# Kernel optimization log

Hardware: AMD Instinct MI355X
Metric: run time of the kernel (lower is better)

## Reference

```python
import math
import jax, jax.numpy as jnp
import numpy as np

B, Q, K, D, H, C = 4, 1024, 1024, 256, 8, 32  # batch, q_len, kv_len, model dim, heads, per-head dim


def setup_inputs() -> dict:
    key = jax.random.key(0)
    ks = jax.random.split(key, 9)
    s = 1.0 / math.sqrt(D)
    return {
        "q_x": jax.random.normal(ks[0], (B, Q, D), jnp.float32),
        "kv_x": jax.random.normal(ks[1], (B, K, D), jnp.float32),
        "bias_mask": jax.random.normal(ks[2], (B, 1, 1, K), jnp.float32),
        "bias_pair": jax.random.normal(ks[3], (B, H, Q, K), jnp.float32),
        "wq": jax.random.normal(ks[4], (D, H * C), jnp.float32) * s,
        "wk": jax.random.normal(ks[5], (D, H * C), jnp.float32) * s,
        "wv": jax.random.normal(ks[6], (D, H * C), jnp.float32) * s,
        "wg": jnp.zeros((D, H * C), jnp.float32),  # gating init: weights 0
        "bg": jnp.ones((H * C,), jnp.float32),     # gating init: bias 1
        "wo": jax.random.normal(ks[7], (H * C, D), jnp.float32) * s,
        "bo": jnp.zeros((D,), jnp.float32),
    }


def reference(q_x, kv_x, bias_mask, bias_pair, wq, wk, wv, wg, bg, wo, bo):
    # project and split heads: [B, L, H, C]
    q = (q_x @ wq).reshape(B, Q, H, C) / math.sqrt(C)
    k = (kv_x @ wk).reshape(B, K, H, C)
    v = (kv_x @ wv).reshape(B, K, H, C)
    # scores [B, H, Q, K] with multiple additive biases
    scores = jnp.einsum("bqhc,bkhc->bhqk", q, k) + bias_mask + bias_pair
    a = jax.nn.softmax(scores, axis=-1)
    o = jnp.einsum("bhqk,bkhc->bqhc", a, v).reshape(B, Q, H * C)
    # sigmoid gate from query activations
    g = jax.nn.sigmoid(q_x @ wg + bg)
    o = o * g
    return o @ wo + bo
```

## Files before the change

### kernel.cpp

```cpp
#include <hip/hip_runtime.h>
#include <hip/hip_bf16.h>


typedef short bf16x8 __attribute__((ext_vector_type(8)));
typedef float f32x4 __attribute__((ext_vector_type(4)));

__device__ __forceinline__ unsigned short f2bf(float f) {
  __hip_bfloat16 hb = __float2bfloat16(f);
  return *reinterpret_cast<const unsigned short*>(&hb);
}

__global__ __launch_bounds__(256) void transpose_conv(
    const float* __restrict__ wq, const float* __restrict__ wk,
    const float* __restrict__ wv, const float* __restrict__ wg,
    const float* __restrict__ wo, unsigned short* __restrict__ wt) {
  __shared__ float t[64][65];
  const int widx = blockIdx.x >> 4;
  const int tile = blockIdx.x & 15;
  const float* src = widx == 0 ? wq : widx == 1 ? wk
                     : widx == 2 ? wv : widx == 3 ? wg : wo;
  unsigned short* dst = wt + widx * 65536;
  const int r0 = (tile >> 2) * 64, c0 = (tile & 3) * 64;
  const int tr = threadIdx.x >> 4;
  const int tc4 = (threadIdx.x & 15) * 4;
#pragma unroll
  for (int i = 0; i < 4; ++i) {
    const float4 u = *reinterpret_cast<const float4*>(
        src + (size_t)(r0 + tr + i * 16) * 256 + c0 + tc4);
    t[tr + i * 16][tc4 + 0] = u.x;
    t[tr + i * 16][tc4 + 1] = u.y;
    t[tr + i * 16][tc4 + 2] = u.z;
    t[tr + i * 16][tc4 + 3] = u.w;
  }
  __syncthreads();
#pragma unroll
  for (int i = 0; i < 4; ++i) {
    const int rr = tr + i * 16;
    ushort4 o;
    o.x = f2bf(t[tc4 + 0][rr]);
    o.y = f2bf(t[tc4 + 1][rr]);
    o.z = f2bf(t[tc4 + 2][rr]);
    o.w = f2bf(t[tc4 + 3][rr]);
    *reinterpret_cast<ushort4*>(dst + (size_t)(c0 + rr) * 256 + r0 + tc4) = o;
  }
}

__global__ __launch_bounds__(256) void proj_mfma(
    const float* __restrict__ q_x, const float* __restrict__ kv_x,
    const unsigned short* __restrict__ wt, const float* __restrict__ bg,
    unsigned short* __restrict__ qhb, unsigned short* __restrict__ khb,
    unsigned short* __restrict__ vhb, float* __restrict__ gws) {
  const int side = blockIdx.y;
  const int m0 = blockIdx.x * 16;
  const int lane = threadIdx.x & 63;
  const int n0 = (threadIdx.x >> 6) * 64;
  const int mrow = lane & 15;
  const int quad = lane >> 4;
  const float* X = side ? kv_x : q_x;
  const unsigned short* W0 = wt + (side ? 1 : 0) * 65536;
  const unsigned short* W1 = wt + (side ? 2 : 3) * 65536;
  f32x4 acc0[4], acc1[4];
  const f32x4 z = {0.f, 0.f, 0.f, 0.f};
#pragma unroll
  for (int nt = 0; nt < 4; ++nt) { acc0[nt] = z; acc1[nt] = z; }

  for (int k0 = 0; k0 < 256; k0 += 32) {
    const size_t abase = (size_t)(m0 + mrow) * 256 + k0 + quad * 8;
    const float4 a0 = *reinterpret_cast<const float4*>(X + abase);
    const float4 a1 = *reinterpret_cast<const float4*>(X + abase + 4);
    bf16x8 a;
    a[0] = (short)f2bf(a0.x); a[1] = (short)f2bf(a0.y);
    a[2] = (short)f2bf(a0.z); a[3] = (short)f2bf(a0.w);
    a[4] = (short)f2bf(a1.x); a[5] = (short)f2bf(a1.y);
    a[6] = (short)f2bf(a1.z); a[7] = (short)f2bf(a1.w);
#pragma unroll
    for (int nt = 0; nt < 4; ++nt) {
      const size_t wrow = (size_t)(n0 + nt * 16 + mrow) * 256 + k0 + quad * 8;
      const bf16x8 b0 = *reinterpret_cast<const bf16x8*>(W0 + wrow);
      const bf16x8 b1 = *reinterpret_cast<const bf16x8*>(W1 + wrow);
      acc0[nt] = __builtin_amdgcn_mfma_f32_16x16x32_bf16(a, b0, acc0[nt], 0, 0, 0);
      acc1[nt] = __builtin_amdgcn_mfma_f32_16x16x32_bf16(a, b1, acc1[nt], 0, 0, 0);
    }
  }

  const int b = m0 >> 10;
#pragma unroll
  for (int nt = 0; nt < 4; ++nt) {
    const int n = n0 + nt * 16 + mrow;
    const int h = n >> 5, c = n & 31;
    const float bgv = (side == 0) ? bg[n] : 0.f;
#pragma unroll
    for (int r = 0; r < 4; ++r) {
      const int row = m0 + quad * 4 + r;
      const int qp = row & 1023;
      const size_t o = ((size_t)(b * 8 + h) * 1024 + qp) * 32 + c;
      if (side == 0) {
        qhb[o] = f2bf(acc0[nt][r] * 0.17677669529663689f);
        const float zz = acc1[nt][r] + bgv;
        gws[(size_t)row * 256 + n] = 1.0f / (1.0f + __expf(-zz));
      } else {
        khb[o] = f2bf(acc0[nt][r]);
        vhb[o] = f2bf(acc1[nt][r]);
      }
    }
  }
}

__global__ __launch_bounds__(256) void attn_mfma(
    const unsigned short* __restrict__ qhb,
    const unsigned short* __restrict__ khb,
    const unsigned short* __restrict__ vhb,
    const float* __restrict__ bias_mask,
    const float* __restrict__ bias_pair,
    const float* __restrict__ gws, unsigned short* __restrict__ og) {
  __shared__ unsigned short ks[64 * 40];
  __shared__ unsigned short vsT[32 * 72];
  __shared__ unsigned short ps[64 * 72];
  const int x = blockIdx.x;
  const int b = x >> 7, h = (x >> 4) & 7, q0 = (x & 15) * 64;
  const int tid = threadIdx.x;
  const int wv = tid >> 6, lane = tid & 63, quad = lane >> 4, lr = lane & 15;
  const int bh = b * 8 + h;

  const bf16x8 aq = *reinterpret_cast<const bf16x8*>(
      qhb + ((size_t)bh * 1024 + q0 + wv * 16 + lr) * 32 + quad * 8);

  float m[4], l[4];
  f32x4 oa[2];
  const f32x4 zero4 = {0.f, 0.f, 0.f, 0.f};
  oa[0] = zero4; oa[1] = zero4;
#pragma unroll
  for (int r = 0; r < 4; ++r) { m[r] = -3e30f; l[r] = 0.f; }

  const float* bp = bias_pair + ((size_t)bh * 1024 + q0 + wv * 16) * 1024;
  const float* bm = bias_mask + (size_t)b * 1024;

  for (int kt = 0; kt < 16; ++kt) {
    const int kk0 = kt * 64;
    __syncthreads();
    {
      const unsigned short* ksrc = khb + (size_t)bh * 32768 + kk0 * 32;
      const int row = tid >> 2, c8 = (tid & 3) * 8;
      *reinterpret_cast<bf16x8*>(ks + row * 40 + c8) =
          *reinterpret_cast<const bf16x8*>(ksrc + row * 32 + c8);
      const unsigned short* vsrc = vhb + (size_t)bh * 32768 + kk0 * 32;
      const bf16x8 vv = *reinterpret_cast<const bf16x8*>(vsrc + row * 32 + c8);
#pragma unroll
      for (int i = 0; i < 8; ++i) vsT[(c8 + i) * 72 + row] = (unsigned short)vv[i];
    }
    __syncthreads();

    f32x4 s[4];
    float mk[4];
#pragma unroll
    for (int nt = 0; nt < 4; ++nt) mk[nt] = bm[kk0 + 16 * nt + lr];
#pragma unroll
    for (int nt = 0; nt < 4; ++nt) {
#pragma unroll
      for (int r = 0; r < 4; ++r)
        s[nt][r] = bp[(size_t)(quad * 4 + r) * 1024 + kk0 + 16 * nt + lr] + mk[nt];
      const bf16x8 bk = *reinterpret_cast<const bf16x8*>(
          ks + (16 * nt + lr) * 40 + quad * 8);
      s[nt] = __builtin_amdgcn_mfma_f32_16x16x32_bf16(aq, bk, s[nt], 0, 0, 0);
    }

#pragma unroll
    for (int r = 0; r < 4; ++r) {
      float mx = fmaxf(fmaxf(s[0][r], s[1][r]), fmaxf(s[2][r], s[3][r]));
      mx = fmaxf(mx, __shfl_xor(mx, 1));
      mx = fmaxf(mx, __shfl_xor(mx, 2));
      mx = fmaxf(mx, __shfl_xor(mx, 4));
      mx = fmaxf(mx, __shfl_xor(mx, 8));
      const float mn = fmaxf(m[r], mx);
      const float alpha = __expf(m[r] - mn);
      float rs = 0.f;
#pragma unroll
      for (int nt = 0; nt < 4; ++nt) {
        s[nt][r] = __expf(s[nt][r] - mn);
        rs += s[nt][r];
      }
      rs += __shfl_xor(rs, 1);
      rs += __shfl_xor(rs, 2);
      rs += __shfl_xor(rs, 4);
      rs += __shfl_xor(rs, 8);
      l[r] = l[r] * alpha + rs;
      m[r] = mn;
      oa[0][r] *= alpha;
      oa[1][r] *= alpha;
      const int ri = wv * 16 + quad * 4 + r;
#pragma unroll
      for (int nt = 0; nt < 4; ++nt)
        ps[ri * 72 + 16 * nt + lr] = f2bf(s[nt][r]);
    }
    asm volatile("s_waitcnt lgkmcnt(0)" ::: "memory");

#pragma unroll
    for (int k0i = 0; k0i < 2; ++k0i) {
      const bf16x8 ap = *reinterpret_cast<const bf16x8*>(
          ps + (wv * 16 + lr) * 72 + k0i * 32 + quad * 8);
#pragma unroll
      for (int nt2 = 0; nt2 < 2; ++nt2) {
        const bf16x8 bv = *reinterpret_cast<const bf16x8*>(
            vsT + (nt2 * 16 + lr) * 72 + k0i * 32 + quad * 8);
        oa[nt2] = __builtin_amdgcn_mfma_f32_16x16x32_bf16(ap, bv, oa[nt2], 0, 0, 0);
      }
    }
  }

#pragma unroll
  for (int r = 0; r < 4; ++r) {
    const int qr = q0 + wv * 16 + quad * 4 + r;
    const float inv = 1.0f / l[r];
    const size_t base = ((size_t)b * 1024 + qr) * 256 + h * 32;
#pragma unroll
    for (int nt2 = 0; nt2 < 2; ++nt2) {
      const int c = nt2 * 16 + lr;
      og[base + c] = f2bf(oa[nt2][r] * inv * gws[base + c]);
    }
  }
}

__global__ __launch_bounds__(256) void outproj_mfma(
    const unsigned short* __restrict__ og,
    const unsigned short* __restrict__ wt,
    const float* __restrict__ bo, float* __restrict__ out) {
  const int m0 = blockIdx.x * 16;
  const int lane = threadIdx.x & 63;
  const int n0 = (threadIdx.x >> 6) * 64;
  const int mrow = lane & 15;
  const int quad = lane >> 4;
  const unsigned short* W = wt + 4 * 65536;
  f32x4 acc[4];
  const f32x4 z = {0.f, 0.f, 0.f, 0.f};
#pragma unroll
  for (int nt = 0; nt < 4; ++nt) acc[nt] = z;

  for (int k0 = 0; k0 < 256; k0 += 32) {
    const bf16x8 a = *reinterpret_cast<const bf16x8*>(
        og + (size_t)(m0 + mrow) * 256 + k0 + quad * 8);
#pragma unroll
    for (int nt = 0; nt < 4; ++nt) {
      const bf16x8 b = *reinterpret_cast<const bf16x8*>(
          W + (size_t)(n0 + nt * 16 + mrow) * 256 + k0 + quad * 8);
      acc[nt] = __builtin_amdgcn_mfma_f32_16x16x32_bf16(a, b, acc[nt], 0, 0, 0);
    }
  }

#pragma unroll
  for (int nt = 0; nt < 4; ++nt) {
    const int n = n0 + nt * 16 + mrow;
    const float bov = bo[n];
#pragma unroll
    for (int r = 0; r < 4; ++r) {
      const int row = m0 + quad * 4 + r;
      out[(size_t)row * 256 + n] = acc[nt][r] + bov;
    }
  }
}

extern "C" void kernel_launch(void* const* d_in, const int* in_sizes, int n_in,
                              void* d_out, int out_size, void* d_ws,
                              size_t ws_size, hipStream_t stream) {
  (void)in_sizes; (void)n_in; (void)out_size; (void)ws_size;
  const float* q_x = (const float*)d_in[0];
  const float* kv_x = (const float*)d_in[1];
  const float* bias_mask = (const float*)d_in[2];
  const float* bias_pair = (const float*)d_in[3];
  const float* wq = (const float*)d_in[4];
  const float* wk = (const float*)d_in[5];
  const float* wv = (const float*)d_in[6];
  const float* wg = (const float*)d_in[7];
  const float* bg = (const float*)d_in[8];
  const float* wo = (const float*)d_in[9];
  const float* bo = (const float*)d_in[10];

  char* wsb = (char*)d_ws;
  unsigned short* wt  = (unsigned short*)(wsb);
  unsigned short* qhb = (unsigned short*)(wsb + 655360);
  unsigned short* khb = (unsigned short*)(wsb + 2752512);
  unsigned short* vhb = (unsigned short*)(wsb + 4849664);
  unsigned short* og  = (unsigned short*)(wsb + 6946816);
  float* gws          = (float*)(wsb + 9043968);

  transpose_conv<<<80, 256, 0, stream>>>(wq, wk, wv, wg, wo, wt);
  proj_mfma<<<dim3(256, 2), 256, 0, stream>>>(q_x, kv_x, wt, bg, qhb, khb,
                                              vhb, gws);
  attn_mfma<<<512, 256, 0, stream>>>(qhb, khb, vhb, bias_mask, bias_pair, gws,
                                     og);
  outproj_mfma<<<256, 256, 0, stream>>>(og, wt, bo, (float*)d_out);
}
```

Baseline: 252.7 us.

## Double-buffer K/V tiles and prefetch bias_pair into registers in attention

The attention kernel now keeps two LDS buffers for K and transposed V. It issues the global loads for the next K/V tile and the next bias_pair/bias_mask values into registers at the start of each iteration, so they overlap the current tile's MFMA and softmax work. This also drops one __syncthreads per iteration. The cost is extra register pressure from holding 16 prefetched bias values plus K/V vectors, which could reduce occupancy.

```diff
diff --git a/kernel.cpp b/kernel.cpp
--- a/kernel.cpp
+++ b/kernel.cpp
@@ -113,8 +113,8 @@
     const float* __restrict__ bias_mask,
     const float* __restrict__ bias_pair,
     const float* __restrict__ gws, unsigned short* __restrict__ og) {
-  __shared__ unsigned short ks[64 * 40];
-  __shared__ unsigned short vsT[32 * 72];
+  __shared__ unsigned short ks[2][64 * 40];
+  __shared__ unsigned short vsT[2][32 * 72];
   __shared__ unsigned short ps[64 * 72];
   const int x = blockIdx.x;
   const int b = x >> 7, h = (x >> 4) & 7, q0 = (x & 15) * 64;
@@ -134,33 +134,53 @@
 
   const float* bp = bias_pair + ((size_t)bh * 1024 + q0 + wv * 16) * 1024;
   const float* bm = bias_mask + (size_t)b * 1024;
+  const unsigned short* kbase = khb + (size_t)bh * 32768;
+  const unsigned short* vbase = vhb + (size_t)bh * 32768;
+  const int srow = tid >> 2, sc8 = (tid & 3) * 8;
+
+  {
+    const bf16x8 k0v = *reinterpret_cast<const bf16x8*>(kbase + srow * 32 + sc8);
+    const bf16x8 v0v = *reinterpret_cast<const bf16x8*>(vbase + srow * 32 + sc8);
+    *reinterpret_cast<bf16x8*>(&ks[0][srow * 40 + sc8]) = k0v;
+#pragma unroll
+    for (int i = 0; i < 8; ++i)
+      vsT[0][(sc8 + i) * 72 + srow] = (unsigned short)v0v[i];
+  }
+  float bpr[4][4], mkr[4];
+#pragma unroll
+  for (int nt = 0; nt < 4; ++nt) {
+    mkr[nt] = bm[16 * nt + lr];
+#pragma unroll
+    for (int r = 0; r < 4; ++r)
+      bpr[nt][r] = bp[(size_t)(quad * 4 + r) * 1024 + 16 * nt + lr];
+  }
+  __syncthreads();
 
   for (int kt = 0; kt < 16; ++kt) {
-    const int kk0 = kt * 64;
-    __syncthreads();
-    {
-      const unsigned short* ksrc = khb + (size_t)bh * 32768 + kk0 * 32;
-      const int row = tid >> 2, c8 = (tid & 3) * 8;
-      *reinterpret_cast<bf16x8*>(ks + row * 40 + c8) =
-          *reinterpret_cast<const bf16x8*>(ksrc + row * 32 + c8);
-      const unsigned short* vsrc = vhb + (size_t)bh * 32768 + kk0 * 32;
-      const bf16x8 vv = *reinterpret_cast<const bf16x8*>(vsrc + row * 32 + c8);
-#pragma unroll
-      for (int i = 0; i < 8; ++i) vsT[(c8 + i) * 72 + row] = (unsigned short)vv[i];
-    }
-    __syncthreads();
+    const int cur = kt & 1;
+
+    bf16x8 kn, vn;
+    float bpn[4][4], mkn[4];
+    if (kt < 15) {
+      const int kk1 = (kt + 1) * 64;
+      kn = *reinterpret_cast<const bf16x8*>(kbase + (size_t)(kk1 + srow) * 32 + sc8);
+      vn = *reinterpret_cast<const bf16x8*>(vbase + (size_t)(kk1 + srow) * 32 + sc8);
+#pragma unroll
+      for (int nt = 0; nt < 4; ++nt) {
+        mkn[nt] = bm[kk1 + 16 * nt + lr];
+#pragma unroll
+        for (int r = 0; r < 4; ++r)
+          bpn[nt][r] = bp[(size_t)(quad * 4 + r) * 1024 + kk1 + 16 * nt + lr];
+      }
+    }
 
     f32x4 s[4];
-    float mk[4];
-#pragma unroll
-    for (int nt = 0; nt < 4; ++nt) mk[nt] = bm[kk0 + 16 * nt + lr];
 #pragma unroll
     for (int nt = 0; nt < 4; ++nt) {
 #pragma unroll
-      for (int r = 0; r < 4; ++r)
-        s[nt][r] = bp[(size_t)(quad * 4 + r) * 1024 + kk0 + 16 * nt + lr] + mk[nt];
+      for (int r = 0; r < 4; ++r) s[nt][r] = bpr[nt][r] + mkr[nt];
       const bf16x8 bk = *reinterpret_cast<const bf16x8*>(
-          ks + (16 * nt + lr) * 40 + quad * 8);
+          &ks[cur][(16 * nt + lr) * 40 + quad * 8]);
       s[nt] = __builtin_amdgcn_mfma_f32_16x16x32_bf16(aq, bk, s[nt], 0, 0, 0);
     }
 
@@ -197,14 +217,28 @@
 #pragma unroll
     for (int k0i = 0; k0i < 2; ++k0i) {
       const bf16x8 ap = *reinterpret_cast<const bf16x8*>(
-          ps + (wv * 16 + lr) * 72 + k0i * 32 + quad * 8);
+          &ps[(wv * 16 + lr) * 72 + k0i * 32 + quad * 8]);
 #pragma unroll
       for (int nt2 = 0; nt2 < 2; ++nt2) {
         const bf16x8 bv = *reinterpret_cast<const bf16x8*>(
-            vsT + (nt2 * 16 + lr) * 72 + k0i * 32 + quad * 8);
+            &vsT[cur][(nt2 * 16 + lr) * 72 + k0i * 32 + quad * 8]);
         oa[nt2] = __builtin_amdgcn_mfma_f32_16x16x32_bf16(ap, bv, oa[nt2], 0, 0, 0);
       }
     }
+
+    if (kt < 15) {
+      *reinterpret_cast<bf16x8*>(&ks[cur ^ 1][srow * 40 + sc8]) = kn;
+#pragma unroll
+      for (int i = 0; i < 8; ++i)
+        vsT[cur ^ 1][(sc8 + i) * 72 + srow] = (unsigned short)vn[i];
+#pragma unroll
+      for (int nt = 0; nt < 4; ++nt) {
+        mkr[nt] = mkn[nt];
+#pragma unroll
+        for (int r = 0; r < 4; ++r) bpr[nt][r] = bpn[nt][r];
+      }
+    }
+    __syncthreads();
   }
 
 #pragma unroll
```

Measured after the change: 255.3 us. Within noise of the previous version (+1.0%).

## Split key range across waves in attention and merge softmax partials in LDS

Applied to the files above, without the earlier changes.

Each attention block now covers 32 queries instead of 64, and the grid doubles to 1024 blocks. Its four waves form two query groups times two key halves. Each pass stages 128 keys into double K/V LDS buffers, and at the end the two key-half partial max, sum and output states are merged through LDS reused from the K buffer. This raises block count and memory-level parallelism for the bandwidth-heavy bias_pair stream. The cost is K/V tiles loaded twice as often per query and an extra merge step with two barriers.

```diff
diff --git a/kernel.cpp b/kernel.cpp
--- a/kernel.cpp
+++ b/kernel.cpp
@@ -113,17 +113,19 @@
     const float* __restrict__ bias_mask,
     const float* __restrict__ bias_pair,
     const float* __restrict__ gws, unsigned short* __restrict__ og) {
-  __shared__ unsigned short ks[64 * 40];
-  __shared__ unsigned short vsT[32 * 72];
+  __shared__ unsigned short ks[2][64 * 40];
+  __shared__ unsigned short vsT[2][32 * 72];
   __shared__ unsigned short ps[64 * 72];
   const int x = blockIdx.x;
-  const int b = x >> 7, h = (x >> 4) & 7, q0 = (x & 15) * 64;
+  const int b = x >> 8, h = (x >> 5) & 7, q0 = (x & 31) * 32;
   const int tid = threadIdx.x;
   const int wv = tid >> 6, lane = tid & 63, quad = lane >> 4, lr = lane & 15;
+  const int qg = wv & 1;
+  const int kp = wv >> 1;
   const int bh = b * 8 + h;
 
   const bf16x8 aq = *reinterpret_cast<const bf16x8*>(
-      qhb + ((size_t)bh * 1024 + q0 + wv * 16 + lr) * 32 + quad * 8);
+      qhb + ((size_t)bh * 1024 + q0 + qg * 16 + lr) * 32 + quad * 8);
 
   float m[4], l[4];
   f32x4 oa[2];
@@ -132,23 +134,29 @@
 #pragma unroll
   for (int r = 0; r < 4; ++r) { m[r] = -3e30f; l[r] = 0.f; }
 
-  const float* bp = bias_pair + ((size_t)bh * 1024 + q0 + wv * 16) * 1024;
+  const float* bp = bias_pair + ((size_t)bh * 1024 + q0 + qg * 16) * 1024;
   const float* bm = bias_mask + (size_t)b * 1024;
-
-  for (int kt = 0; kt < 16; ++kt) {
-    const int kk0 = kt * 64;
+  const unsigned short* kbase = khb + (size_t)bh * 32768;
+  const unsigned short* vbase = vhb + (size_t)bh * 32768;
+
+  for (int i = 0; i < 8; ++i) {
     __syncthreads();
-    {
-      const unsigned short* ksrc = khb + (size_t)bh * 32768 + kk0 * 32;
-      const int row = tid >> 2, c8 = (tid & 3) * 8;
-      *reinterpret_cast<bf16x8*>(ks + row * 40 + c8) =
-          *reinterpret_cast<const bf16x8*>(ksrc + row * 32 + c8);
-      const unsigned short* vsrc = vhb + (size_t)bh * 32768 + kk0 * 32;
-      const bf16x8 vv = *reinterpret_cast<const bf16x8*>(vsrc + row * 32 + c8);
-#pragma unroll
-      for (int i = 0; i < 8; ++i) vsT[(c8 + i) * 72 + row] = (unsigned short)vv[i];
+#pragma unroll
+    for (int j = 0; j < 2; ++j) {
+      const int ch = tid * 2 + j;
+      const int rr = ch >> 2, c8 = (ch & 3) * 8;
+      const int p = rr >> 6, r64 = rr & 63;
+      const size_t src = (size_t)(i * 128 + rr) * 32 + c8;
+      *reinterpret_cast<bf16x8*>(&ks[p][r64 * 40 + c8]) =
+          *reinterpret_cast<const bf16x8*>(kbase + src);
+      const bf16x8 vvv = *reinterpret_cast<const bf16x8*>(vbase + src);
+#pragma unroll
+      for (int j2 = 0; j2 < 8; ++j2)
+        vsT[p][(c8 + j2) * 72 + r64] = (unsigned short)vvv[j2];
     }
     __syncthreads();
+
+    const int kk0 = (i * 2 + kp) * 64;
 
     f32x4 s[4];
     float mk[4];
@@ -160,7 +168,7 @@
       for (int r = 0; r < 4; ++r)
         s[nt][r] = bp[(size_t)(quad * 4 + r) * 1024 + kk0 + 16 * nt + lr] + mk[nt];
       const bf16x8 bk = *reinterpret_cast<const bf16x8*>(
-          ks + (16 * nt + lr) * 40 + quad * 8);
+          &ks[kp][(16 * nt + lr) * 40 + quad * 8]);
       s[nt] = __builtin_amdgcn_mfma_f32_16x16x32_bf16(aq, bk, s[nt], 0, 0, 0);
     }
 
@@ -197,25 +205,47 @@
 #pragma unroll
     for (int k0i = 0; k0i < 2; ++k0i) {
       const bf16x8 ap = *reinterpret_cast<const bf16x8*>(
-          ps + (wv * 16 + lr) * 72 + k0i * 32 + quad * 8);
+          &ps[(wv * 16 + lr) * 72 + k0i * 32 + quad * 8]);
 #pragma unroll
       for (int nt2 = 0; nt2 < 2; ++nt2) {
         const bf16x8 bv = *reinterpret_cast<const bf16x8*>(
-            vsT + (nt2 * 16 + lr) * 72 + k0i * 32 + quad * 8);
+            &vsT[kp][(nt2 * 16 + lr) * 72 + k0i * 32 + quad * 8]);
         oa[nt2] = __builtin_amdgcn_mfma_f32_16x16x32_bf16(ap, bv, oa[nt2], 0, 0, 0);
       }
     }
   }
 
-#pragma unroll
-  for (int r = 0; r < 4; ++r) {
-    const int qr = q0 + wv * 16 + quad * 4 + r;
-    const float inv = 1.0f / l[r];
-    const size_t base = ((size_t)b * 1024 + qr) * 256 + h * 32;
-#pragma unroll
-    for (int nt2 = 0; nt2 < 2; ++nt2) {
-      const int c = nt2 * 16 + lr;
-      og[base + c] = f2bf(oa[nt2][r] * inv * gws[base + c]);
+  float* mrg = reinterpret_cast<float*>(ks);
+  __syncthreads();
+  if (kp == 1) {
+    const int base = (qg * 64 + lane) * 16;
+#pragma unroll
+    for (int r = 0; r < 4; ++r) {
+      mrg[base + r] = m[r];
+      mrg[base + 4 + r] = l[r];
+      mrg[base + 8 + r] = oa[0][r];
+      mrg[base + 12 + r] = oa[1][r];
+    }
+  }
+  __syncthreads();
+  if (kp == 0) {
+    const int base = (qg * 64 + lane) * 16;
+#pragma unroll
+    for (int r = 0; r < 4; ++r) {
+      const float pm = mrg[base + r];
+      const float pl = mrg[base + 4 + r];
+      const float po0 = mrg[base + 8 + r];
+      const float po1 = mrg[base + 12 + r];
+      const float mn = fmaxf(m[r], pm);
+      const float a0 = __expf(m[r] - mn);
+      const float a1 = __expf(pm - mn);
+      const float inv = 1.0f / (l[r] * a0 + pl * a1);
+      const int qr = q0 + qg * 16 + quad * 4 + r;
+      const size_t obase = ((size_t)b * 1024 + qr) * 256 + h * 32;
+      const float o0 = oa[0][r] * a0 + po0 * a1;
+      og[obase + lr] = f2bf(o0 * inv * gws[obase + lr]);
+      const float o1 = oa[1][r] * a0 + po1 * a1;
+      og[obase + 16 + lr] = f2bf(o1 * inv * gws[obase + 16 + lr]);
     }
   }
 }
@@ -285,7 +315,7 @@
   transpose_conv<<<80, 256, 0, stream>>>(wq, wk, wv, wg, wo, wt);
   proj_mfma<<<dim3(256, 2), 256, 0, stream>>>(q_x, kv_x, wt, bg, qhb, khb,
                                               vhb, gws);
-  attn_mfma<<<512, 256, 0, stream>>>(qhb, khb, vhb, bias_mask, bias_pair, gws,
-                                     og);
+  attn_mfma<<<1024, 256, 0, stream>>>(qhb, khb, vhb, bias_mask, bias_pair,
+                                      gws, og);
   outproj_mfma<<<256, 256, 0, stream>>>(og, wt, bo, (float*)d_out);
 }
```

Result: no change. 251.0 us (-0.7%).
